# Optimization experiments

Measured on AMD Instinct MI355X. Metric: run time of the kernel, lower is better.

The kernel has to match this reference:

```python
import jax, jax.numpy as jnp
import numpy as np

B, P, K = 32, 1024, 16  # clouds, points per cloud, neighbors


def setup_inputs() -> dict:
    key = jax.random.key(0)
    ks = jax.random.split(key, 5)
    N, C, H, D = B * P, 64, 128, 3
    x = jax.random.normal(ks[0], (N, C), dtype=jnp.float32)
    pos = jax.random.normal(ks[1], (N, D), dtype=jnp.float32)
    batch = jnp.arange(N, dtype=jnp.int64) // P  # cloud id per node
    W_e = jax.random.normal(ks[2], (2 * C, H), dtype=jnp.float32) * 0.05
    b_e = jnp.zeros((H,), dtype=jnp.float32)
    W_sc = jax.random.normal(ks[3], (C, H), dtype=jnp.float32) * 0.05
    b_sc = jnp.zeros((H,), dtype=jnp.float32)
    return {"x": x, "pos": pos, "batch": batch,
            "W_e": W_e, "b_e": b_e, "W_sc": W_sc, "b_sc": b_sc}


def _knn_idx(posb):
    # posb: [B, P, D] -> idx [B, P, K]: K nearest neighbors (sources) per target node,
    # within each cloud, excluding self (loop=False in torch_geometric.knn_graph).
    sq = jnp.sum(posb * posb, axis=-1)                       # [B, P]
    d2 = sq[:, :, None] + sq[:, None, :] - 2.0 * jnp.einsum('bid,bjd->bij', posb, posb)
    d2 = d2 + jnp.eye(P, dtype=posb.dtype)[None] * jnp.finfo(posb.dtype).max / 2
    _, idx = jax.lax.top_k(-d2, K)                           # [B, P, K]
    return idx


def reference(x, pos, batch, W_e, b_e, W_sc, b_sc):
    C = x.shape[-1]
    xb = x.reshape(B, P, C)
    posb = pos.reshape(B, P, -1)
    idx = _knn_idx(posb)                                     # [B, P, K]
    # gather neighbor (source) features per target node
    x_j = jax.vmap(lambda xc, ic: xc[ic])(xb, idx)           # [B, P, K, C]
    x_i = xb[:, :, None, :]                                  # [B, P, 1, C]
    # EdgeConv message: nn([x_i, x_j - x_i]), here Linear + ReLU
    e = jnp.concatenate([jnp.broadcast_to(x_i, x_j.shape), x_j - x_i], axis=-1)  # [B,P,K,2C]
    msg = jax.nn.relu(jnp.einsum('bpke,eh->bpkh', e, W_e) + b_e)
    agg = jnp.max(msg, axis=2)                               # max aggregation -> [B, P, H]
    shortcut = x @ W_sc + b_sc                               # [N, H]
    out = agg.reshape(-1, agg.shape[-1]) + shortcut
    return out
```

## Files before the change

kernel.cpp:

```cpp
#include <hip/hip_runtime.h>
#include <float.h>
#include <stdint.h>

#define BATCHES 32
#define P 1024
#define KNN 16
#define C 64
#define H 128
#define N (BATCHES * P)
#define SPLITS 8
#define CPS 128
#define QB 32
#define PADH 136

typedef short short8 __attribute__((ext_vector_type(8)));
typedef float floatx4 __attribute__((ext_vector_type(4)));

struct alignas(16) F4 { float x, y, z, w; };

__device__ __forceinline__ unsigned short f2bf(float f) {
    unsigned u = __float_as_uint(f);
    unsigned r = (u + 0x7FFF + ((u >> 16) & 1)) >> 16;
    return (unsigned short)r;
}

__global__ __launch_bounds__(256) void prep_kernel(
    const float* __restrict__ W_e, const float* __restrict__ b_e,
    const float* __restrict__ W_sc, const float* __restrict__ b_sc,
    const float* __restrict__ X,
    unsigned short* __restrict__ WT, float* __restrict__ bias,
    unsigned short* __restrict__ V)
{
    __shared__ unsigned short Vs[128][PADH];
    int b = blockIdx.x;
    int t = threadIdx.x;
    if (b < 96) {
        int i = b * 256 + t;
        int col = i >> 6, c = i & 63;
        float w;
        if (col < 128)      w = W_e[c * 128 + col] - W_e[(64 + c) * 128 + col];
        else if (col < 256) w = W_e[(64 + c) * 128 + (col - 128)];
        else                w = W_sc[c * 128 + (col - 256)];
        WT[col * 64 + c] = f2bf(w);
        if (c == 0) {
            bias[col] = (col < 128) ? b_e[col] : (col < 256 ? 0.0f : b_sc[col - 256]);
        }
        return;
    }

    int vb = b - 96;
    int m0 = vb * 128;
    int w  = t >> 6, ln = t & 63;
    int lm = ln & 15, kg = ln >> 4;

    short8 a0[2], a1[2];
#pragma unroll
    for (int i = 0; i < 2; ++i) {
        int row = m0 + (2 * w + i) * 16 + lm;
        const float4* ar = (const float4*)(X + (size_t)row * 64 + kg * 8);
        float4 f0 = ar[0], f1 = ar[1], f2 = ar[8], f3 = ar[9];
        a0[i][0] = (short)f2bf(f0.x); a0[i][1] = (short)f2bf(f0.y);
        a0[i][2] = (short)f2bf(f0.z); a0[i][3] = (short)f2bf(f0.w);
        a0[i][4] = (short)f2bf(f1.x); a0[i][5] = (short)f2bf(f1.y);
        a0[i][6] = (short)f2bf(f1.z); a0[i][7] = (short)f2bf(f1.w);
        a1[i][0] = (short)f2bf(f2.x); a1[i][1] = (short)f2bf(f2.y);
        a1[i][2] = (short)f2bf(f2.z); a1[i][3] = (short)f2bf(f2.w);
        a1[i][4] = (short)f2bf(f3.x); a1[i][5] = (short)f2bf(f3.y);
        a1[i][6] = (short)f2bf(f3.z); a1[i][7] = (short)f2bf(f3.w);
    }

#pragma unroll 2
    for (int ct = 0; ct < 8; ++ct) {
        int col = ct * 16 + lm;
        short8 b0, b1;
#pragma unroll
        for (int i = 0; i < 8; ++i) {
            b0[i] = (short)f2bf(W_e[(size_t)(64 + kg * 8 + i) * 128 + col]);
            b1[i] = (short)f2bf(W_e[(size_t)(96 + kg * 8 + i) * 128 + col]);
        }
#pragma unroll
        for (int i = 0; i < 2; ++i) {
            floatx4 acc = {0.0f, 0.0f, 0.0f, 0.0f};
            acc = __builtin_amdgcn_mfma_f32_16x16x32_bf16(a0[i], b0, acc, 0, 0, 0);
            acc = __builtin_amdgcn_mfma_f32_16x16x32_bf16(a1[i], b1, acc, 0, 0, 0);
#pragma unroll
            for (int r = 0; r < 4; ++r)
                Vs[(2 * w + i) * 16 + kg * 4 + r][col] = f2bf(acc[r]);
        }
    }
    __syncthreads();

    uint2* Vg = (uint2*)V + (size_t)vb * 4096;
#pragma unroll
    for (int i = t; i < 4096; i += 256) {
        int row = i >> 5, off = (i & 31) * 4;
        Vg[i] = *(const uint2*)&Vs[row][off];
    }
}

struct SM {
    F4 spos[P + 8];
    union {
        struct {
            float lists[SPLITS][16][QB];
            unsigned short offs[SPLITS][QB];
            unsigned short cnts[SPLITS][QB];
            float Tq[QB];
        };
        struct {
            unsigned short Ubuf[QB][PADH];
            unsigned short Sbuf[QB][PADH];
        };
    };
    int nbr[QB][KNN];
};

__global__ __launch_bounds__(256, 4) void knn_gemm_kernel(
    const float* __restrict__ pos, const float* __restrict__ X,
    const unsigned short* __restrict__ WT, const float* __restrict__ bias,
    const unsigned short* __restrict__ V,
    float* __restrict__ out)
{
    __shared__ __align__(16) SM A;

    int t = threadIdx.x;
    int q = t & 31, s = t >> 5;
    int blk = blockIdx.x;
    int batch = blk >> 5;
    int qblk  = blk & 31;
    int iloc  = qblk * QB + q;

    const float* pb = pos + (size_t)batch * P * 3;
    for (int j = t; j < P; j += 256) {
        float x = pb[j * 3 + 0], y = pb[j * 3 + 1], z = pb[j * 3 + 2];
        float sq = __fadd_rn(__fadd_rn(__fmul_rn(x, x), __fmul_rn(y, y)),
                             __fmul_rn(z, z));
        A.spos[j] = F4{x, y, z, sq};
    }
    __syncthreads();

    F4 me = A.spos[iloc];
    const int j0 = s * CPS;

    float d[16];
#pragma unroll
    for (int k = 0; k < 16; ++k) d[k] = FLT_MAX;

    auto dist = [&](const F4& c, int j) -> float {
        float dot = __fadd_rn(__fadd_rn(__fmul_rn(me.x, c.x), __fmul_rn(me.y, c.y)),
                              __fmul_rn(me.z, c.z));
        float d2 = __fadd_rn(__fadd_rn(me.w, c.w), __fmul_rn(-2.0f, dot));
        return (j == iloc) ? FLT_MAX : d2;
    };
    auto insert = [&](float d2) {
#pragma unroll
        for (int k = 15; k >= 1; --k)
            d[k] = __builtin_amdgcn_fmed3f(d[k - 1], d2, d[k]);
        d[0] = fminf(d[0], d2);
    };

#pragma unroll 8
    for (int jj = 0; jj < CPS; ++jj) {
        int j = j0 + jj;
        F4 c = A.spos[j];
        insert(dist(c, j));
    }

#pragma unroll
    for (int k = 0; k < 16; ++k) A.lists[s][k][q] = d[k];
    __syncthreads();

    if ((t >> 6) == (blk & 3) && (t & 63) < QB) {
        int qm = t & 63;
        float v[8], wv[8];
        int   n[8];
#pragma unroll
        for (int l = 0; l < 8; ++l) {
            v[l]  = A.lists[l][0][qm];
            wv[l] = A.lists[l][1][qm];
            n[l]  = 0;
        }
        float T = 0.0f;
#pragma unroll 1
        for (int k = 0; k < 16; ++k) {
            float mn = fminf(fminf(fminf(v[0], v[1]), fminf(v[2], v[3])),
                             fminf(fminf(v[4], v[5]), fminf(v[6], v[7])));
            bool taken = false;
#pragma unroll
            for (int l = 0; l < 8; ++l) {
                bool tk = (!taken) && (v[l] == mn);
                taken = taken || tk;
                int ni = n[l] + (tk ? 1 : 0);
                int ri = ni + 1;
                float rv = A.lists[l][(ri < 16) ? ri : 15][qm];
                float wnew = (ri < 16) ? rv : FLT_MAX;
                v[l]  = tk ? wv[l] : v[l];
                wv[l] = tk ? wnew  : wv[l];
                n[l]  = ni;
            }
            T = mn;
        }
        A.Tq[qm] = T;
        int off = 0;
#pragma unroll
        for (int l = 0; l < 8; ++l) {
            A.offs[l][qm] = (unsigned short)off;
            A.cnts[l][qm] = (unsigned short)n[l];
            off += n[l];
        }
    }
    __syncthreads();

    {
        float T  = A.Tq[q];
        int   cap = A.cnts[s][q];
        int   ob  = A.offs[s][q];
        int   base = batch * P;
        int   cnt = 0;

#pragma unroll 4
        for (int jj = 0; jj < CPS; ++jj) {
            int j = j0 + jj;
            F4 c = A.spos[j];
            float d2 = dist(c, j);
            if (d2 <= T && cnt < cap) {
                A.nbr[q][ob + cnt] = base + j;
                cnt++;
            }
        }
    }
    __syncthreads();

    {
        int w  = t >> 6;
        int ln = t & 63;
        int mt = w & 1, nh = w >> 1;
        int m0 = blk * QB + mt * 16;
        int lm = ln & 15, kg = ln >> 4;

        const float4* arow = (const float4*)(X + (size_t)(m0 + lm) * 64 + kg * 8);
        float4 f0 = arow[0], f1 = arow[1];
        float4 f2 = arow[8], f3 = arow[9];
        short8 a0, a1;
        a0[0] = (short)f2bf(f0.x); a0[1] = (short)f2bf(f0.y);
        a0[2] = (short)f2bf(f0.z); a0[3] = (short)f2bf(f0.w);
        a0[4] = (short)f2bf(f1.x); a0[5] = (short)f2bf(f1.y);
        a0[6] = (short)f2bf(f1.z); a0[7] = (short)f2bf(f1.w);
        a1[0] = (short)f2bf(f2.x); a1[1] = (short)f2bf(f2.y);
        a1[2] = (short)f2bf(f2.z); a1[3] = (short)f2bf(f2.w);
        a1[4] = (short)f2bf(f3.x); a1[5] = (short)f2bf(f3.y);
        a1[6] = (short)f2bf(f3.z); a1[7] = (short)f2bf(f3.w);

        int tbase = (nh == 0) ? 0 : 16;
#pragma unroll 4
        for (int nt = tbase; nt < tbase + 8; ++nt) {
            const short8* brow = (const short8*)(WT + (size_t)(nt * 16 + lm) * 64 + kg * 8);
            short8 b0 = brow[0];
            short8 b1 = brow[4];
            floatx4 acc = {0.0f, 0.0f, 0.0f, 0.0f};
            acc = __builtin_amdgcn_mfma_f32_16x16x32_bf16(a0, b0, acc, 0, 0, 0);
            acc = __builtin_amdgcn_mfma_f32_16x16x32_bf16(a1, b1, acc, 0, 0, 0);

            int col = nt * 16 + lm;
            float bv = bias[col];
#pragma unroll
            for (int r = 0; r < 4; ++r) {
                int row = mt * 16 + kg * 4 + r;
                unsigned short val = f2bf(acc[r] + bv);
                if (col < 128) A.Ubuf[row][col] = val;
                else           A.Sbuf[row][col - 256] = val;
            }
        }
    }
    __syncthreads();

    {
        int pl = t >> 4;
        int c8 = t & 15;
#pragma unroll
        for (int half = 0; half < 2; ++half) {
            int q2 = half * 16 + pl;
            size_t p = (size_t)blk * QB + q2;

            uint4 uu = *(const uint4*)&A.Ubuf[q2][c8 * 8];
            uint4 ss = *(const uint4*)&A.Sbuf[q2][c8 * 8];

            float m0 = -FLT_MAX, m1 = -FLT_MAX, m2 = -FLT_MAX, m3 = -FLT_MAX;
            float m4 = -FLT_MAX, m5 = -FLT_MAX, m6 = -FLT_MAX, m7 = -FLT_MAX;
#pragma unroll
            for (int k = 0; k < KNN; ++k) {
                int row = A.nbr[q2][k];
                uint4 vv = *(const uint4*)(V + (size_t)row * H + c8 * 8);
                m0 = fmaxf(m0, __uint_as_float(vv.x << 16));
                m1 = fmaxf(m1, __uint_as_float(vv.x & 0xFFFF0000u));
                m2 = fmaxf(m2, __uint_as_float(vv.y << 16));
                m3 = fmaxf(m3, __uint_as_float(vv.y & 0xFFFF0000u));
                m4 = fmaxf(m4, __uint_as_float(vv.z << 16));
                m5 = fmaxf(m5, __uint_as_float(vv.z & 0xFFFF0000u));
                m6 = fmaxf(m6, __uint_as_float(vv.w << 16));
                m7 = fmaxf(m7, __uint_as_float(vv.w & 0xFFFF0000u));
            }

            float4 oa, ob;
            oa.x = fmaxf(__uint_as_float(uu.x << 16)         + m0, 0.0f) + __uint_as_float(ss.x << 16);
            oa.y = fmaxf(__uint_as_float(uu.x & 0xFFFF0000u) + m1, 0.0f) + __uint_as_float(ss.x & 0xFFFF0000u);
            oa.z = fmaxf(__uint_as_float(uu.y << 16)         + m2, 0.0f) + __uint_as_float(ss.y << 16);
            oa.w = fmaxf(__uint_as_float(uu.y & 0xFFFF0000u) + m3, 0.0f) + __uint_as_float(ss.y & 0xFFFF0000u);
            ob.x = fmaxf(__uint_as_float(uu.z << 16)         + m4, 0.0f) + __uint_as_float(ss.z << 16);
            ob.y = fmaxf(__uint_as_float(uu.z & 0xFFFF0000u) + m5, 0.0f) + __uint_as_float(ss.z & 0xFFFF0000u);
            ob.z = fmaxf(__uint_as_float(uu.w << 16)         + m6, 0.0f) + __uint_as_float(ss.w << 16);
            ob.w = fmaxf(__uint_as_float(uu.w & 0xFFFF0000u) + m7, 0.0f) + __uint_as_float(ss.w & 0xFFFF0000u);
            ((float4*)(out + p * H))[c8 * 2]     = oa;
            ((float4*)(out + p * H))[c8 * 2 + 1] = ob;
        }
    }
}

extern "C" void kernel_launch(void* const* d_in, const int* in_sizes, int n_in,
                              void* d_out, int out_size, void* d_ws, size_t ws_size,
                              hipStream_t stream)
{
    const float* x    = (const float*)d_in[0];
    const float* pos  = (const float*)d_in[1];
    const float* W_e  = (const float*)d_in[3];
    const float* b_e  = (const float*)d_in[4];
    const float* W_sc = (const float*)d_in[5];
    const float* b_sc = (const float*)d_in[6];
    float* out = (float*)d_out;

    char* ws = (char*)d_ws;
    const size_t OFF_V    = 0;
    const size_t OFF_WT   = 8ull << 20;
    const size_t OFF_BIAS = OFF_WT + 49152;

    unsigned short* V    = (unsigned short*)(ws + OFF_V);
    unsigned short* WT   = (unsigned short*)(ws + OFF_WT);
    float*          bias = (float*)(ws + OFF_BIAS);

    prep_kernel<<<96 + N / 128, 256, 0, stream>>>(W_e, b_e, W_sc, b_sc, x,
                                                  WT, bias, V);
    knn_gemm_kernel<<<N / QB, 256, 0, stream>>>(pos, x, WT, bias, V, out);
}
```

Before: 132.5 us.

## Double query block to 64 with 512-thread blocks; precompute pos+norm in prep kernel

Moves the per-point position and squared-norm packing into the prep kernel, which writes it to a global workspace buffer. The kNN kernel now reads candidate positions from global memory (wave-uniform, so broadcast through the cache) instead of staging them in LDS. Blocks grow to 512 threads covering 64 queries, which halves the number of blocks and redundant per-batch work but changes occupancy. Reading candidates from global instead of LDS risks higher load latency in the hot distance loop.

```diff
diff --git a/kernel.cpp b/kernel.cpp
--- a/kernel.cpp
+++ b/kernel.cpp
@@ -10,7 +10,7 @@
 #define N (BATCHES * P)
 #define SPLITS 8
 #define CPS 128
-#define QB 32
+#define QB 64
 #define PADH 136
 
 typedef short short8 __attribute__((ext_vector_type(8)));
@@ -27,9 +27,9 @@
 __global__ __launch_bounds__(256) void prep_kernel(
     const float* __restrict__ W_e, const float* __restrict__ b_e,
     const float* __restrict__ W_sc, const float* __restrict__ b_sc,
-    const float* __restrict__ X,
+    const float* __restrict__ X, const float* __restrict__ pos,
     unsigned short* __restrict__ WT, float* __restrict__ bias,
-    unsigned short* __restrict__ V)
+    F4* __restrict__ posq, unsigned short* __restrict__ V)
 {
     __shared__ unsigned short Vs[128][PADH];
     int b = blockIdx.x;
@@ -47,8 +47,16 @@
         }
         return;
     }
-
-    int vb = b - 96;
+    if (b < 224) {
+        int j = (b - 96) * 256 + t;
+        float x = pos[j * 3 + 0], y = pos[j * 3 + 1], z = pos[j * 3 + 2];
+        float sq = __fadd_rn(__fadd_rn(__fmul_rn(x, x), __fmul_rn(y, y)),
+                             __fmul_rn(z, z));
+        posq[j] = F4{x, y, z, sq};
+        return;
+    }
+
+    int vb = b - 224;
     int m0 = vb * 128;
     int w  = t >> 6, ln = t & 63;
     int lm = ln & 15, kg = ln >> 4;
@@ -99,7 +107,6 @@
 }
 
 struct SM {
-    F4 spos[P + 8];
     union {
         struct {
             float lists[SPLITS][16][QB];
@@ -115,8 +122,8 @@
     int nbr[QB][KNN];
 };
 
-__global__ __launch_bounds__(256, 4) void knn_gemm_kernel(
-    const float* __restrict__ pos, const float* __restrict__ X,
+__global__ __launch_bounds__(512, 2) void knn_gemm_kernel(
+    const F4* __restrict__ posq, const float* __restrict__ X,
     const unsigned short* __restrict__ WT, const float* __restrict__ bias,
     const unsigned short* __restrict__ V,
     float* __restrict__ out)
@@ -124,23 +131,16 @@
     __shared__ __align__(16) SM A;
 
     int t = threadIdx.x;
-    int q = t & 31, s = t >> 5;
+    int q = t & 63;
+    int su = __builtin_amdgcn_readfirstlane(t >> 6);
     int blk = blockIdx.x;
-    int batch = blk >> 5;
-    int qblk  = blk & 31;
+    int batch = blk >> 4;
+    int qblk  = blk & 15;
     int iloc  = qblk * QB + q;
 
-    const float* pb = pos + (size_t)batch * P * 3;
-    for (int j = t; j < P; j += 256) {
-        float x = pb[j * 3 + 0], y = pb[j * 3 + 1], z = pb[j * 3 + 2];
-        float sq = __fadd_rn(__fadd_rn(__fmul_rn(x, x), __fmul_rn(y, y)),
-                             __fmul_rn(z, z));
-        A.spos[j] = F4{x, y, z, sq};
-    }
-    __syncthreads();
-
-    F4 me = A.spos[iloc];
-    const int j0 = s * CPS;
+    const F4* pq = posq + (size_t)batch * P;
+    F4 me = pq[iloc];
+    const int j0 = su * CPS;
 
     float d[16];
 #pragma unroll
@@ -159,25 +159,24 @@
         d[0] = fminf(d[0], d2);
     };
 
-#pragma unroll 8
+#pragma unroll 4
     for (int jj = 0; jj < CPS; ++jj) {
         int j = j0 + jj;
-        F4 c = A.spos[j];
+        F4 c = pq[j];
         insert(dist(c, j));
     }
 
 #pragma unroll
-    for (int k = 0; k < 16; ++k) A.lists[s][k][q] = d[k];
-    __syncthreads();
-
-    if ((t >> 6) == (blk & 3) && (t & 63) < QB) {
-        int qm = t & 63;
+    for (int k = 0; k < 16; ++k) A.lists[su][k][q] = d[k];
+    __syncthreads();
+
+    if (su == (blk & 7)) {
         float v[8], wv[8];
         int   n[8];
 #pragma unroll
         for (int l = 0; l < 8; ++l) {
-            v[l]  = A.lists[l][0][qm];
-            wv[l] = A.lists[l][1][qm];
+            v[l]  = A.lists[l][0][q];
+            wv[l] = A.lists[l][1][q];
             n[l]  = 0;
         }
         float T = 0.0f;
@@ -192,7 +191,7 @@
                 taken = taken || tk;
                 int ni = n[l] + (tk ? 1 : 0);
                 int ri = ni + 1;
-                float rv = A.lists[l][(ri < 16) ? ri : 15][qm];
+                float rv = A.lists[l][(ri < 16) ? ri : 15][q];
                 float wnew = (ri < 16) ? rv : FLT_MAX;
                 v[l]  = tk ? wv[l] : v[l];
                 wv[l] = tk ? wnew  : wv[l];
@@ -200,12 +199,12 @@
             }
             T = mn;
         }
-        A.Tq[qm] = T;
+        A.Tq[q] = T;
         int off = 0;
 #pragma unroll
         for (int l = 0; l < 8; ++l) {
-            A.offs[l][qm] = (unsigned short)off;
-            A.cnts[l][qm] = (unsigned short)n[l];
+            A.offs[l][q] = (unsigned short)off;
+            A.cnts[l][q] = (unsigned short)n[l];
             off += n[l];
         }
     }
@@ -213,15 +212,15 @@
 
     {
         float T  = A.Tq[q];
-        int   cap = A.cnts[s][q];
-        int   ob  = A.offs[s][q];
+        int   cap = A.cnts[su][q];
+        int   ob  = A.offs[su][q];
         int   base = batch * P;
         int   cnt = 0;
 
 #pragma unroll 4
         for (int jj = 0; jj < CPS; ++jj) {
             int j = j0 + jj;
-            F4 c = A.spos[j];
+            F4 c = pq[j];
             float d2 = dist(c, j);
             if (d2 <= T && cnt < cap) {
                 A.nbr[q][ob + cnt] = base + j;
@@ -234,7 +233,7 @@
     {
         int w  = t >> 6;
         int ln = t & 63;
-        int mt = w & 1, nh = w >> 1;
+        int mt = w & 3, nh = w >> 2;
         int m0 = blk * QB + mt * 16;
         int lm = ln & 15, kg = ln >> 4;
 
@@ -279,7 +278,7 @@
         int c8 = t & 15;
 #pragma unroll
         for (int half = 0; half < 2; ++half) {
-            int q2 = half * 16 + pl;
+            int q2 = half * 32 + pl;
             size_t p = (size_t)blk * QB + q2;
 
             uint4 uu = *(const uint4*)&A.Ubuf[q2][c8 * 8];
@@ -332,12 +331,14 @@
     const size_t OFF_V    = 0;
     const size_t OFF_WT   = 8ull << 20;
     const size_t OFF_BIAS = OFF_WT + 49152;
+    const size_t OFF_POSQ = OFF_BIAS + 2048;
 
     unsigned short* V    = (unsigned short*)(ws + OFF_V);
     unsigned short* WT   = (unsigned short*)(ws + OFF_WT);
     float*          bias = (float*)(ws + OFF_BIAS);
-
-    prep_kernel<<<96 + N / 128, 256, 0, stream>>>(W_e, b_e, W_sc, b_sc, x,
-                                                  WT, bias, V);
-    knn_gemm_kernel<<<N / QB, 256, 0, stream>>>(pos, x, WT, bias, V, out);
+    F4*             posq = (F4*)(ws + OFF_POSQ);
+
+    prep_kernel<<<224 + N / 128, 256, 0, stream>>>(W_e, b_e, W_sc, b_sc, x, pos,
+                                                   WT, bias, posq, V);
+    knn_gemm_kernel<<<N / QB, 512, 0, stream>>>(posq, x, WT, bias, V, out);
 }
```

After: 138.2 us. 1.04x slower.
